# Optimization experiments

Hardware: AMD Instinct MI355X
Metric: run time of the kernel (lower is better)

The kernel has to match this reference:

```python
import jax, jax.numpy as jnp
import numpy as np
import math

L, H, P = 16384, 128, 256


def setup_inputs() -> dict:
    key = jax.random.key(0)
    k = jax.random.split(key, 6)
    return {
        "input_sequence": jax.random.normal(k[0], (L, H), dtype=jnp.float32),
        "A_diag": jax.random.uniform(k[1], (P,), dtype=jnp.float32),
        "B": (jax.random.uniform(k[2], (P, H, 2), dtype=jnp.float32) * 2.0 - 1.0) / math.sqrt(H),
        "C": (jax.random.uniform(k[3], (H, P, 2), dtype=jnp.float32) * 2.0 - 1.0) / math.sqrt(P),
        "D": jax.random.normal(k[4], (H,), dtype=jnp.float32),
        "steps": jax.random.uniform(k[5], (P,), dtype=jnp.float32),
    }


def _binop(qi, qj):
    # 2x2 block-diagonal matrix product + affine state propagation, per channel.
    iA, iB, iC, iD, ib1, ib2 = qi
    jA, jB, jC, jD, jb1, jb2 = qj
    return (
        jA * iA + jB * iC,
        jA * iB + jB * iD,
        jC * iA + jD * iC,
        jC * iB + jD * iD,
        jA * ib1 + jB * ib2 + jb1,
        jC * ib1 + jD * ib2 + jb2,
    )


def reference(input_sequence, A_diag, B, C, D, steps):
    # LinOSS-IM discretization (implicit)
    A = jax.nn.relu(A_diag)                      # (P,)
    dt = jax.nn.sigmoid(steps)                   # (P,)
    Bc = B[..., 0] + 1j * B[..., 1]              # (P,H) complex64
    Cc = C[..., 0] + 1j * C[..., 1]              # (H,P) complex64

    Bu = input_sequence @ Bc.T                   # (L,P) complex64

    schur = 1.0 / (1.0 + dt ** 2 * A)
    M11 = 1.0 - dt ** 2 * A * schur
    M12 = -dt * A * schur
    M21 = dt * schur
    M22 = schur

    ones = jnp.ones((input_sequence.shape[0], A.shape[0]), dtype=input_sequence.dtype)
    F1 = M11 * Bu * dt                           # (L,P) complex
    F2 = M21 * Bu * dt

    elems = (M11 * ones, M12 * ones, M21 * ones, M22 * ones, F1, F2)
    _, _, _, _, _, x2 = jax.lax.associative_scan(_binop, elems)  # scan over L

    ys = jnp.real(x2 @ Cc.T)                     # (L,H)
    return ys + input_sequence * D
```

## Files before the change

kernel.cpp:

```cpp
#include <hip/hip_runtime.h>
#include <hip/hip_bf16.h>
#include <math.h>

#define L 16384
#define H 128
#define P 256
#define CL 32
#define NCH (L/CL)
#define GS 16
#define NG (NCH/GS)
#define KDIM 512
#define NBU 512

typedef __attribute__((ext_vector_type(8))) short short8;
typedef __attribute__((ext_vector_type(4))) float f32x4;

__device__ inline unsigned short f2bf(float f){
  union { float f; unsigned u; } v; v.f = f;
  unsigned u = v.u;
  u += 0x7fffu + ((u >> 16) & 1u);
  return (unsigned short)(u >> 16);
}
__device__ inline float bf2f(unsigned short s){
  union { unsigned u; float f; } v; v.u = ((unsigned)s) << 16;
  return v.f;
}

struct Params { float M11,M12,M21,M22,s1,s2; };

__device__ inline Params get_params(const float* A_diag, const float* steps, int p){
  float A = A_diag[p]; A = A > 0.f ? A : 0.f;
  float dt = 1.f/(1.f + expf(-steps[p]));
  float schur = 1.f/(1.f + dt*dt*A);
  Params q;
  q.M11 = 1.f - dt*dt*A*schur;
  q.M12 = -dt*A*schur;
  q.M21 = dt*schur;
  q.M22 = schur;
  q.s1 = q.M11*dt;
  q.s2 = q.M21*dt;
  return q;
}

__global__ __launch_bounds__(256) void cast_in(const float* __restrict__ in,
                                               unsigned short* __restrict__ inb){
  int i = blockIdx.x * 256 + threadIdx.x;
  const float4* g = (const float4*)in;
  float4 a = g[i*2], b = g[i*2+1];
  union { short8 s; unsigned short u[8]; } o;
  o.u[0]=f2bf(a.x); o.u[1]=f2bf(a.y); o.u[2]=f2bf(a.z); o.u[3]=f2bf(a.w);
  o.u[4]=f2bf(b.x); o.u[5]=f2bf(b.y); o.u[6]=f2bf(b.z); o.u[7]=f2bf(b.w);
  ((short8*)inb)[i] = o.s;
}

__global__ __launch_bounds__(512) void bwswz_prep(const float* __restrict__ B,
                                                  unsigned short* __restrict__ BWswz){
  int k = blockIdx.x;
  int n = threadIdx.x;
  int p = n & 255, c = n >> 8;
  float v = B[((size_t)p*H + k)*2 + c];
  BWswz[((size_t)(k>>3)*NBU + n)*8 + (k&7)] = f2bf(v);
}

__global__ __launch_bounds__(128) void bswz_prep(const float* __restrict__ C,
                                                 unsigned short* __restrict__ Bswz){
  int k = blockIdx.x;
  int n = threadIdx.x;
  float v = (k < P) ? C[((size_t)n*P + k)*2]
                    : -C[((size_t)n*P + (k-P))*2 + 1];
  Bswz[((size_t)(k>>3)*H + n)*8 + (k&7)] = f2bf(v);
}

__device__ inline void chunk_bu_to_lds(int c, const short* __restrict__ inb,
                                       const short* __restrict__ BWswz,
                                       unsigned short (*sBu)[NBU+8]){
  int tid = threadIdx.x;
  int lane = tid & 63, w = tid >> 6;
  int ml = lane & 15, quad = lane >> 4;
  int mt = w & 1, ng = w >> 1;
  int lm0 = mt*16;
  const short* aptr = inb + (size_t)(c*CL + lm0 + ml)*H + quad*8;
  short8 av[4];
  #pragma unroll
  for (int ks=0; ks<4; ks++) av[ks] = *(const short8*)(aptr + ks*32);
  f32x4 acc[8];
  #pragma unroll
  for (int t=0;t<8;t++) acc[t] = (f32x4){0.f,0.f,0.f,0.f};
  #pragma unroll
  for (int ks=0; ks<4; ks++){
    #pragma unroll
    for (int t=0;t<8;t++){
      int n0 = (ng*8 + t)*16;
      short8 bv = *(const short8*)(BWswz + ((size_t)(ks*4+quad)*NBU + n0 + ml)*8);
      acc[t] = __builtin_amdgcn_mfma_f32_16x16x32_bf16(av[ks], bv, acc[t], 0, 0, 0);
    }
  }
  #pragma unroll
  for (int t=0;t<8;t++){
    int n = (ng*8+t)*16 + ml;
    #pragma unroll
    for (int r=0;r<4;r++)
      sBu[lm0 + quad*4 + r][n] = f2bf(acc[t][r]);
  }
}

__global__ __launch_bounds__(512) void bu_finals(const short* __restrict__ inb,
                                                 const short* __restrict__ BWswz,
                                                 const float* __restrict__ A_diag,
                                                 const float* __restrict__ steps,
                                                 float* __restrict__ finals){
  __shared__ unsigned short sBu[CL][NBU+8];
  int c = blockIdx.x;
  chunk_bu_to_lds(c, inb, BWswz, sBu);
  __syncthreads();
  int tid = threadIdx.x;
  int p = tid & 255, part = tid >> 8;
  Params q = get_params(A_diag, steps, p);
  float x1=0.f, x2=0.f;
  #pragma unroll
  for (int i=0;i<CL;i++){
    float u = bf2f(sBu[i][part*256 + p]);
    float n1 = q.M11*x1 + q.M12*x2 + q.s1*u;
    float n2 = q.M21*x1 + q.M22*x2 + q.s2*u;
    x1 = n1; x2 = n2;
  }
  ((float2*)finals)[(size_t)(part*NCH + c)*P + p] = make_float2(x1,x2);
}

__global__ __launch_bounds__(512) void group_scan(const float* __restrict__ A_diag,
                                                  const float* __restrict__ steps,
                                                  float* zf,
                                                  float* __restrict__ gfin){
  int tid = threadIdx.x;
  int p = tid & (P-1);
  int part = tid >> 8;
  int g = blockIdx.x;
  Params q = get_params(A_diag, steps, p);
  float a=q.M11, b=q.M12, c=q.M21, d=q.M22;
  #pragma unroll
  for (int s=0;s<5;s++){
    float na=a*a+b*c, nb=a*b+b*d, nc=c*a+d*c, nd=c*b+d*d;
    a=na;b=nb;c=nc;d=nd;
  }
  float2* z2 = (float2*)zf;
  float x1=0.f, x2=0.f;
  #pragma unroll
  for (int i=0;i<GS;i++){
    size_t idx = (size_t)(part*NCH + g*GS + i)*P + p;
    float2 f = z2[idx];
    z2[idx] = make_float2(x1,x2);
    float n1 = a*x1 + b*x2 + f.x;
    float n2 = c*x1 + d*x2 + f.y;
    x1=n1; x2=n2;
  }
  ((float2*)gfin)[(size_t)(part*NG + g)*P + p] = make_float2(x1,x2);
}

__global__ __launch_bounds__(512) void group_combine(const float* __restrict__ A_diag,
                                                     const float* __restrict__ steps,
                                                     const float* __restrict__ gfin,
                                                     float* __restrict__ Yarr){
  int tid = threadIdx.x;
  int p = tid & (P-1);
  int part = tid >> 8;
  Params q = get_params(A_diag, steps, p);
  float a=q.M11, b=q.M12, c=q.M21, d=q.M22;
  #pragma unroll
  for (int s=0;s<9;s++){
    float na=a*a+b*c, nb=a*b+b*d, nc=c*a+d*c, nd=c*b+d*d;
    a=na;b=nb;c=nc;d=nd;
  }
  const float2* Z2 = (const float2*)gfin;
  float2* Y2 = (float2*)Yarr;
  float x1=0.f, x2=0.f;
  #pragma unroll
  for (int g=0; g<NG; g++){
    size_t idx = (size_t)(part*NG + g)*P + p;
    Y2[idx] = make_float2(x1,x2);
    float2 z = Z2[idx];
    float n1 = a*x1 + b*x2 + z.x;
    float n2 = c*x1 + d*x2 + z.y;
    x1=n1; x2=n2;
  }
}

__global__ __launch_bounds__(512) void fused_out(const short* __restrict__ inb,
                                                 const short* __restrict__ BWswz,
                                                 const short* __restrict__ Bswz,
                                                 const float* __restrict__ A_diag,
                                                 const float* __restrict__ steps,
                                                 const float* __restrict__ zloc,
                                                 const float* __restrict__ Yarr,
                                                 const float* __restrict__ Dv,
                                                 const float* __restrict__ in,
                                                 float* __restrict__ out){
  __shared__ unsigned short sX[CL][KDIM+8];
  int c = blockIdx.x;
  chunk_bu_to_lds(c, inb, BWswz, sX);
  __syncthreads();

  int tid = threadIdx.x;
  {
    int p = tid & 255, part = tid >> 8;
    int g = c >> 4, iw = c & (GS-1);
    Params q = get_params(A_diag, steps, p);
    float a=q.M11, b=q.M12, cc=q.M21, dd=q.M22;
    #pragma unroll
    for (int s=0;s<5;s++){
      float na=a*a+b*cc, nb=a*b+b*dd, nc=cc*a+dd*cc, nd=cc*b+dd*dd;
      a=na;b=nb;cc=nc;dd=nd;
    }
    float sa=1.f, sb=0.f, sc=0.f, sd=1.f;
    float wa=a, wb=b, wc=cc, wd=dd;
    #pragma unroll
    for (int bit=0; bit<4; bit++){
      if ((iw>>bit)&1){
        float na = wa*sa + wb*sc, nb = wa*sb + wb*sd;
        float nc = wc*sa + wd*sc, nd = wc*sb + wd*sd;
        sa=na; sb=nb; sc=nc; sd=nd;
      }
      float qa = wa*wa + wb*wc, qb = wa*wb + wb*wd;
      float qc = wc*wa + wd*wc, qd = wc*wb + wd*wd;
      wa=qa; wb=qb; wc=qc; wd=qd;
    }
    float2 Y = ((const float2*)Yarr)[(size_t)(part*NG + g)*P + p];
    float2 z = ((const float2*)zloc)[(size_t)(part*NCH + c)*P + p];
    float x1 = sa*Y.x + sb*Y.y + z.x;
    float x2 = sc*Y.x + sd*Y.y + z.y;
    #pragma unroll
    for (int i=0;i<CL;i++){
      float u = bf2f(sX[i][part*256 + p]);
      float n1 = q.M11*x1 + q.M12*x2 + q.s1*u;
      float n2 = q.M21*x1 + q.M22*x2 + q.s2*u;
      x1 = n1; x2 = n2;
      sX[i][part*256 + p] = f2bf(x2);
    }
  }
  __syncthreads();

  int lane = tid & 63, w = tid >> 6;
  int ml = lane & 15, quad = lane >> 4;
  int mt = w & 1;
  int ntb = (w >> 1) * 2;
  f32x4 acc[2];
  acc[0] = (f32x4){0.f,0.f,0.f,0.f};
  acc[1] = (f32x4){0.f,0.f,0.f,0.f};
  for (int ks=0; ks<KDIM/32; ks++){
    short8 av = *(const short8*)&sX[mt*16 + ml][ks*32 + quad*8];
    #pragma unroll
    for (int j=0;j<2;j++){
      short8 bv = *(const short8*)(Bswz + ((size_t)(ks*4+quad)*H + (ntb+j)*16 + ml)*8);
      acc[j] = __builtin_amdgcn_mfma_f32_16x16x32_bf16(av, bv, acc[j], 0, 0, 0);
    }
  }
  #pragma unroll
  for (int j=0;j<2;j++){
    int h = (ntb+j)*16 + ml;
    float dv = Dv[h];
    #pragma unroll
    for (int r=0;r<4;r++){
      int l = c*CL + mt*16 + quad*4 + r;
      out[(size_t)l*H + h] = acc[j][r] + in[(size_t)l*H + h]*dv;
    }
  }
}

extern "C" void kernel_launch(void* const* d_in, const int* in_sizes, int n_in,
                              void* d_out, int out_size, void* d_ws, size_t ws_size,
                              hipStream_t stream) {
  const float* in     = (const float*)d_in[0];
  const float* A_diag = (const float*)d_in[1];
  const float* B      = (const float*)d_in[2];
  const float* Cw     = (const float*)d_in[3];
  const float* Dv     = (const float*)d_in[4];
  const float* steps  = (const float*)d_in[5];
  float* out = (float*)d_out;

  unsigned short* inb  = (unsigned short*)d_ws;
  unsigned short* BWswz= inb + (size_t)L*H;
  unsigned short* Bswz = BWswz + (size_t)H*NBU;
  float* finals = (float*)(Bswz + (size_t)KDIM*H);
  float* gfin   = finals + (size_t)2*NCH*P*2;
  float* Yarr   = gfin + (size_t)2*NG*P*2;

  cast_in<<<(L*H)/(8*256), 256, 0, stream>>>(in, inb);
  bwswz_prep<<<H, 512, 0, stream>>>(B, BWswz);
  bswz_prep<<<KDIM, 128, 0, stream>>>(Cw, Bswz);
  bu_finals<<<NCH, 512, 0, stream>>>((const short*)inb, (const short*)BWswz,
                                     A_diag, steps, finals);
  group_scan<<<NG, 512, 0, stream>>>(A_diag, steps, finals, gfin);
  group_combine<<<1, 512, 0, stream>>>(A_diag, steps, gfin, Yarr);
  fused_out<<<NCH, 512, 0, stream>>>((const short*)inb, (const short*)BWswz,
                                     (const short*)Bswz, A_diag, steps,
                                     finals, Yarr, Dv, in, out);
}
```

Before: 109.2 us.

## Merge all stages into one cooperative persistent kernel with grid syncs

Replaces the seven separate launches (cast/prep, chunk finals, group scan, group combine, fused output) with a single cooperative kernel that separates the phases with grid.sync(). The Bu tile stays in LDS between the chunk-finals phase and the output phase, so the output phase no longer recomputes the Bu GEMM. It also removes per-launch gaps. The trade-off is that 512 blocks of 512 threads must all be co-resident for the cooperative launch to succeed, and grid-wide barriers add cost. If the launch fails, the old multi-kernel path runs instead.

Result: slower. 325.5 us (+198.1%).

```diff
diff --git a/kernel.cpp b/kernel.cpp
--- a/kernel.cpp
+++ b/kernel.cpp
@@ -1,6 +1,8 @@
 #include <hip/hip_runtime.h>
-#include <hip/hip_bf16.h>
+#include <hip/hip_cooperative_groups.h>
 #include <math.h>
+
+namespace cg = cooperative_groups;
 
 #define L 16384
 #define H 128
@@ -42,6 +44,208 @@
   return q;
 }
 
+__device__ inline void chunk_bu_to_lds(int c, const short* __restrict__ inb,
+                                       const short* __restrict__ BWswz,
+                                       unsigned short (*sBu)[NBU+8]){
+  int tid = threadIdx.x;
+  int lane = tid & 63, w = tid >> 6;
+  int ml = lane & 15, quad = lane >> 4;
+  int mt = w & 1, ng = w >> 1;
+  int lm0 = mt*16;
+  const short* aptr = inb + (size_t)(c*CL + lm0 + ml)*H + quad*8;
+  short8 av[4];
+  #pragma unroll
+  for (int ks=0; ks<4; ks++) av[ks] = *(const short8*)(aptr + ks*32);
+  f32x4 acc[8];
+  #pragma unroll
+  for (int t=0;t<8;t++) acc[t] = (f32x4){0.f,0.f,0.f,0.f};
+  #pragma unroll
+  for (int ks=0; ks<4; ks++){
+    #pragma unroll
+    for (int t=0;t<8;t++){
+      int n0 = (ng*8 + t)*16;
+      short8 bv = *(const short8*)(BWswz + ((size_t)(ks*4+quad)*NBU + n0 + ml)*8);
+      acc[t] = __builtin_amdgcn_mfma_f32_16x16x32_bf16(av[ks], bv, acc[t], 0, 0, 0);
+    }
+  }
+  #pragma unroll
+  for (int t=0;t<8;t++){
+    int n = (ng*8+t)*16 + ml;
+    #pragma unroll
+    for (int r=0;r<4;r++)
+      sBu[lm0 + quad*4 + r][n] = f2bf(acc[t][r]);
+  }
+}
+
+__global__ __launch_bounds__(512, 4) void linoss_mega(
+    const float* __restrict__ in, const float* __restrict__ A_diag,
+    const float* __restrict__ B, const float* __restrict__ Cw,
+    const float* __restrict__ Dv, const float* __restrict__ steps,
+    unsigned short* __restrict__ inb, unsigned short* __restrict__ BWswz,
+    unsigned short* __restrict__ Bswz, float* finals,
+    float* __restrict__ gfin, float* __restrict__ Yarr,
+    float* __restrict__ out){
+  cg::grid_group grid = cg::this_grid();
+  __shared__ unsigned short sX[CL][NBU+8];
+  int tid = threadIdx.x;
+  int c = blockIdx.x;
+
+  {
+    int gid = c*512 + tid;
+    const float4* g = (const float4*)in;
+    float4 a = g[gid*2], b4 = g[gid*2+1];
+    union { short8 s; unsigned short u[8]; } o;
+    o.u[0]=f2bf(a.x); o.u[1]=f2bf(a.y); o.u[2]=f2bf(a.z); o.u[3]=f2bf(a.w);
+    o.u[4]=f2bf(b4.x); o.u[5]=f2bf(b4.y); o.u[6]=f2bf(b4.z); o.u[7]=f2bf(b4.w);
+    ((short8*)inb)[gid] = o.s;
+    if (gid < H*NBU){
+      int k = gid >> 9, n = gid & 511;
+      int p = n & 255, c2 = n >> 8;
+      float v = B[((size_t)p*H + k)*2 + c2];
+      BWswz[((size_t)(k>>3)*NBU + n)*8 + (k&7)] = f2bf(v);
+    }
+    if (gid < KDIM*H){
+      int k = gid >> 7, n = gid & 127;
+      float v = (k < P) ? Cw[((size_t)n*P + k)*2]
+                        : -Cw[((size_t)n*P + (k-P))*2 + 1];
+      Bswz[((size_t)(k>>3)*H + n)*8 + (k&7)] = f2bf(v);
+    }
+  }
+  grid.sync();
+
+  chunk_bu_to_lds(c, (const short*)inb, (const short*)BWswz, sX);
+  __syncthreads();
+  {
+    int p = tid & 255, part = tid >> 8;
+    Params q = get_params(A_diag, steps, p);
+    float x1=0.f, x2=0.f;
+    #pragma unroll
+    for (int i=0;i<CL;i++){
+      float u = bf2f(sX[i][part*256 + p]);
+      float n1 = q.M11*x1 + q.M12*x2 + q.s1*u;
+      float n2 = q.M21*x1 + q.M22*x2 + q.s2*u;
+      x1 = n1; x2 = n2;
+    }
+    ((float2*)finals)[(size_t)(part*NCH + c)*P + p] = make_float2(x1,x2);
+  }
+  grid.sync();
+
+  if (c < NG){
+    int p = tid & 255, part = tid >> 8;
+    int g = c;
+    Params q = get_params(A_diag, steps, p);
+    float a=q.M11, b=q.M12, cc=q.M21, d=q.M22;
+    #pragma unroll
+    for (int s=0;s<5;s++){
+      float na=a*a+b*cc, nb=a*b+b*d, nc=cc*a+d*cc, nd=cc*b+d*d;
+      a=na;b=nb;cc=nc;d=nd;
+    }
+    float2* z2 = (float2*)finals;
+    float x1=0.f, x2=0.f;
+    #pragma unroll
+    for (int i=0;i<GS;i++){
+      size_t idx = (size_t)(part*NCH + g*GS + i)*P + p;
+      float2 f = z2[idx];
+      z2[idx] = make_float2(x1,x2);
+      float n1 = a*x1 + b*x2 + f.x;
+      float n2 = cc*x1 + d*x2 + f.y;
+      x1=n1; x2=n2;
+    }
+    ((float2*)gfin)[(size_t)(part*NG + g)*P + p] = make_float2(x1,x2);
+  }
+  grid.sync();
+
+  if (c == 0){
+    int p = tid & 255, part = tid >> 8;
+    Params q = get_params(A_diag, steps, p);
+    float a=q.M11, b=q.M12, cc=q.M21, d=q.M22;
+    #pragma unroll
+    for (int s=0;s<9;s++){
+      float na=a*a+b*cc, nb=a*b+b*d, nc=cc*a+d*cc, nd=cc*b+d*d;
+      a=na;b=nb;cc=nc;d=nd;
+    }
+    const float2* Z2 = (const float2*)gfin;
+    float2* Y2 = (float2*)Yarr;
+    float x1=0.f, x2=0.f;
+    #pragma unroll
+    for (int g=0; g<NG; g++){
+      size_t idx = (size_t)(part*NG + g)*P + p;
+      Y2[idx] = make_float2(x1,x2);
+      float2 z = Z2[idx];
+      float n1 = a*x1 + b*x2 + z.x;
+      float n2 = cc*x1 + d*x2 + z.y;
+      x1=n1; x2=n2;
+    }
+  }
+  grid.sync();
+
+  {
+    int p = tid & 255, part = tid >> 8;
+    int g = c >> 4, iw = c & (GS-1);
+    Params q = get_params(A_diag, steps, p);
+    float a=q.M11, b=q.M12, cc=q.M21, dd=q.M22;
+    #pragma unroll
+    for (int s=0;s<5;s++){
+      float na=a*a+b*cc, nb=a*b+b*dd, nc=cc*a+dd*cc, nd=cc*b+dd*dd;
+      a=na;b=nb;cc=nc;dd=nd;
+    }
+    float sa=1.f, sb=0.f, sc=0.f, sd=1.f;
+    float wa=a, wb=b, wc=cc, wd=dd;
+    #pragma unroll
+    for (int bit=0; bit<4; bit++){
+      if ((iw>>bit)&1){
+        float na = wa*sa + wb*sc, nb = wa*sb + wb*sd;
+        float nc = wc*sa + wd*sc, nd = wc*sb + wd*sd;
+        sa=na; sb=nb; sc=nc; sd=nd;
+      }
+      float qa = wa*wa + wb*wc, qb = wa*wb + wb*wd;
+      float qc = wc*wa + wd*wc, qd = wc*wb + wd*wd;
+      wa=qa; wb=qb; wc=qc; wd=qd;
+    }
+    float2 Y = ((const float2*)Yarr)[(size_t)(part*NG + g)*P + p];
+    float2 z = ((const float2*)finals)[(size_t)(part*NCH + c)*P + p];
+    float x1 = sa*Y.x + sb*Y.y + z.x;
+    float x2 = sc*Y.x + sd*Y.y + z.y;
+    #pragma unroll
+    for (int i=0;i<CL;i++){
+      float u = bf2f(sX[i][part*256 + p]);
+      float n1 = q.M11*x1 + q.M12*x2 + q.s1*u;
+      float n2 = q.M21*x1 + q.M22*x2 + q.s2*u;
+      x1 = n1; x2 = n2;
+      sX[i][part*256 + p] = f2bf(x2);
+    }
+  }
+  __syncthreads();
+  {
+    int lane = tid & 63, w = tid >> 6;
+    int ml = lane & 15, quad = lane >> 4;
+    int mt = w & 1;
+    int ntb = (w >> 1) * 2;
+    f32x4 acc[2];
+    acc[0] = (f32x4){0.f,0.f,0.f,0.f};
+    acc[1] = (f32x4){0.f,0.f,0.f,0.f};
+    for (int ks=0; ks<KDIM/32; ks++){
+      short8 av = *(const short8*)&sX[mt*16 + ml][ks*32 + quad*8];
+      #pragma unroll
+      for (int j=0;j<2;j++){
+        short8 bv = *(const short8*)((const short*)Bswz +
+                      ((size_t)(ks*4+quad)*H + (ntb+j)*16 + ml)*8);
+        acc[j] = __builtin_amdgcn_mfma_f32_16x16x32_bf16(av, bv, acc[j], 0, 0, 0);
+      }
+    }
+    #pragma unroll
+    for (int j=0;j<2;j++){
+      int h = (ntb+j)*16 + ml;
+      float dv = Dv[h];
+      #pragma unroll
+      for (int r=0;r<4;r++){
+        int l = c*CL + mt*16 + quad*4 + r;
+        out[(size_t)l*H + h] = acc[j][r] + in[(size_t)l*H + h]*dv;
+      }
+    }
+  }
+}
+
 __global__ __launch_bounds__(256) void cast_in(const float* __restrict__ in,
                                                unsigned short* __restrict__ inb){
   int i = blockIdx.x * 256 + threadIdx.x;
@@ -69,39 +273,6 @@
   float v = (k < P) ? C[((size_t)n*P + k)*2]
                     : -C[((size_t)n*P + (k-P))*2 + 1];
   Bswz[((size_t)(k>>3)*H + n)*8 + (k&7)] = f2bf(v);
-}
-
-__device__ inline void chunk_bu_to_lds(int c, const short* __restrict__ inb,
-                                       const short* __restrict__ BWswz,
-                                       unsigned short (*sBu)[NBU+8]){
-  int tid = threadIdx.x;
-  int lane = tid & 63, w = tid >> 6;
-  int ml = lane & 15, quad = lane >> 4;
-  int mt = w & 1, ng = w >> 1;
-  int lm0 = mt*16;
-  const short* aptr = inb + (size_t)(c*CL + lm0 + ml)*H + quad*8;
-  short8 av[4];
-  #pragma unroll
-  for (int ks=0; ks<4; ks++) av[ks] = *(const short8*)(aptr + ks*32);
-  f32x4 acc[8];
-  #pragma unroll
-  for (int t=0;t<8;t++) acc[t] = (f32x4){0.f,0.f,0.f,0.f};
-  #pragma unroll
-  for (int ks=0; ks<4; ks++){
-    #pragma unroll
-    for (int t=0;t<8;t++){
-      int n0 = (ng*8 + t)*16;
-      short8 bv = *(const short8*)(BWswz + ((size_t)(ks*4+quad)*NBU + n0 + ml)*8);
-      acc[t] = __builtin_amdgcn_mfma_f32_16x16x32_bf16(av[ks], bv, acc[t], 0, 0, 0);
-    }
-  }
-  #pragma unroll
-  for (int t=0;t<8;t++){
-    int n = (ng*8+t)*16 + ml;
-    #pragma unroll
-    for (int r=0;r<4;r++)
-      sBu[lm0 + quad*4 + r][n] = f2bf(acc[t][r]);
-  }
 }
 
 __global__ __launch_bounds__(512) void bu_finals(const short* __restrict__ inb,
@@ -198,7 +369,6 @@
   int c = blockIdx.x;
   chunk_bu_to_lds(c, inb, BWswz, sX);
   __syncthreads();
-
   int tid = threadIdx.x;
   {
     int p = tid & 255, part = tid >> 8;
@@ -237,7 +407,6 @@
     }
   }
   __syncthreads();
-
   int lane = tid & 63, w = tid >> 6;
   int ml = lane & 15, quad = lane >> 4;
   int mt = w & 1;
@@ -283,14 +452,24 @@
   float* gfin   = finals + (size_t)2*NCH*P*2;
   float* Yarr   = gfin + (size_t)2*NG*P*2;
 
-  cast_in<<<(L*H)/(8*256), 256, 0, stream>>>(in, inb);
-  bwswz_prep<<<H, 512, 0, stream>>>(B, BWswz);
-  bswz_prep<<<KDIM, 128, 0, stream>>>(Cw, Bswz);
-  bu_finals<<<NCH, 512, 0, stream>>>((const short*)inb, (const short*)BWswz,
-                                     A_diag, steps, finals);
-  group_scan<<<NG, 512, 0, stream>>>(A_diag, steps, finals, gfin);
-  group_combine<<<1, 512, 0, stream>>>(A_diag, steps, gfin, Yarr);
-  fused_out<<<NCH, 512, 0, stream>>>((const short*)inb, (const short*)BWswz,
-                                     (const short*)Bswz, A_diag, steps,
-                                     finals, Yarr, Dv, in, out);
-}
+  void* args[] = {
+    (void*)&in, (void*)&A_diag, (void*)&B, (void*)&Cw, (void*)&Dv, (void*)&steps,
+    (void*)&inb, (void*)&BWswz, (void*)&Bswz,
+    (void*)&finals, (void*)&gfin, (void*)&Yarr, (void*)&out
+  };
+  hipError_t err = hipLaunchCooperativeKernel((const void*)linoss_mega,
+                                              dim3(NCH), dim3(512),
+                                              args, 0, stream);
+  if (err != hipSuccess) {
+    cast_in<<<(L*H)/(8*256), 256, 0, stream>>>(in, inb);
+    bwswz_prep<<<H, 512, 0, stream>>>(B, BWswz);
+    bswz_prep<<<KDIM, 128, 0, stream>>>(Cw, Bswz);
+    bu_finals<<<NCH, 512, 0, stream>>>((const short*)inb, (const short*)BWswz,
+                                       A_diag, steps, finals);
+    group_scan<<<NG, 512, 0, stream>>>(A_diag, steps, finals, gfin);
+    group_combine<<<1, 512, 0, stream>>>(A_diag, steps, gfin, Yarr);
+    fused_out<<<NCH, 512, 0, stream>>>((const short*)inb, (const short*)BWswz,
+                                       (const short*)Bswz, A_diag, steps,
+                                       finals, Yarr, Dv, in, out);
+  }
+}
```

## Merge prep kernels into one launch and fold group combine into output kernel

Applied to the files above, without the earlier changes.

Combines the three preparation kernels (input cast, B swizzle, C swizzle) into a single launch with 512 blocks. It also drops the single-block group_combine kernel. Each block of fused_out now recomputes its group carry-in by serially scanning up to 31 group finals with the 16th power of the transition matrix. This cuts two launches and removes a serial single-block kernel, at the cost of redundant per-block scan work and extra global reads in fused_out.

Result: faster. 104.3 us (-4.4%).

```diff
diff --git a/kernel.cpp b/kernel.cpp
--- a/kernel.cpp
+++ b/kernel.cpp
@@ -1,5 +1,4 @@
 #include <hip/hip_runtime.h>
-#include <hip/hip_bf16.h>
 #include <math.h>
 
 #define L 16384
@@ -42,33 +41,31 @@
   return q;
 }
 
-__global__ __launch_bounds__(256) void cast_in(const float* __restrict__ in,
-                                               unsigned short* __restrict__ inb){
-  int i = blockIdx.x * 256 + threadIdx.x;
+__global__ __launch_bounds__(512) void prep_all(const float* __restrict__ in,
+                                                const float* __restrict__ B,
+                                                const float* __restrict__ Cw,
+                                                unsigned short* __restrict__ inb,
+                                                unsigned short* __restrict__ BWswz,
+                                                unsigned short* __restrict__ Bswz){
+  int gid = blockIdx.x*512 + threadIdx.x;
   const float4* g = (const float4*)in;
-  float4 a = g[i*2], b = g[i*2+1];
+  float4 a = g[gid*2], b4 = g[gid*2+1];
   union { short8 s; unsigned short u[8]; } o;
   o.u[0]=f2bf(a.x); o.u[1]=f2bf(a.y); o.u[2]=f2bf(a.z); o.u[3]=f2bf(a.w);
-  o.u[4]=f2bf(b.x); o.u[5]=f2bf(b.y); o.u[6]=f2bf(b.z); o.u[7]=f2bf(b.w);
-  ((short8*)inb)[i] = o.s;
-}
-
-__global__ __launch_bounds__(512) void bwswz_prep(const float* __restrict__ B,
-                                                  unsigned short* __restrict__ BWswz){
-  int k = blockIdx.x;
-  int n = threadIdx.x;
-  int p = n & 255, c = n >> 8;
-  float v = B[((size_t)p*H + k)*2 + c];
-  BWswz[((size_t)(k>>3)*NBU + n)*8 + (k&7)] = f2bf(v);
-}
-
-__global__ __launch_bounds__(128) void bswz_prep(const float* __restrict__ C,
-                                                 unsigned short* __restrict__ Bswz){
-  int k = blockIdx.x;
-  int n = threadIdx.x;
-  float v = (k < P) ? C[((size_t)n*P + k)*2]
-                    : -C[((size_t)n*P + (k-P))*2 + 1];
-  Bswz[((size_t)(k>>3)*H + n)*8 + (k&7)] = f2bf(v);
+  o.u[4]=f2bf(b4.x); o.u[5]=f2bf(b4.y); o.u[6]=f2bf(b4.z); o.u[7]=f2bf(b4.w);
+  ((short8*)inb)[gid] = o.s;
+  if (gid < H*NBU){
+    int k = gid >> 9, n = gid & 511;
+    int p = n & 255, c2 = n >> 8;
+    float v = B[((size_t)p*H + k)*2 + c2];
+    BWswz[((size_t)(k>>3)*NBU + n)*8 + (k&7)] = f2bf(v);
+  }
+  if (gid < KDIM*H){
+    int k = gid >> 7, n = gid & 127;
+    float v = (k < P) ? Cw[((size_t)n*P + k)*2]
+                      : -Cw[((size_t)n*P + (k-P))*2 + 1];
+    Bswz[((size_t)(k>>3)*H + n)*8 + (k&7)] = f2bf(v);
+  }
 }
 
 __device__ inline void chunk_bu_to_lds(int c, const short* __restrict__ inb,
@@ -156,41 +153,13 @@
   ((float2*)gfin)[(size_t)(part*NG + g)*P + p] = make_float2(x1,x2);
 }
 
-__global__ __launch_bounds__(512) void group_combine(const float* __restrict__ A_diag,
-                                                     const float* __restrict__ steps,
-                                                     const float* __restrict__ gfin,
-                                                     float* __restrict__ Yarr){
-  int tid = threadIdx.x;
-  int p = tid & (P-1);
-  int part = tid >> 8;
-  Params q = get_params(A_diag, steps, p);
-  float a=q.M11, b=q.M12, c=q.M21, d=q.M22;
-  #pragma unroll
-  for (int s=0;s<9;s++){
-    float na=a*a+b*c, nb=a*b+b*d, nc=c*a+d*c, nd=c*b+d*d;
-    a=na;b=nb;c=nc;d=nd;
-  }
-  const float2* Z2 = (const float2*)gfin;
-  float2* Y2 = (float2*)Yarr;
-  float x1=0.f, x2=0.f;
-  #pragma unroll
-  for (int g=0; g<NG; g++){
-    size_t idx = (size_t)(part*NG + g)*P + p;
-    Y2[idx] = make_float2(x1,x2);
-    float2 z = Z2[idx];
-    float n1 = a*x1 + b*x2 + z.x;
-    float n2 = c*x1 + d*x2 + z.y;
-    x1=n1; x2=n2;
-  }
-}
-
 __global__ __launch_bounds__(512) void fused_out(const short* __restrict__ inb,
                                                  const short* __restrict__ BWswz,
                                                  const short* __restrict__ Bswz,
                                                  const float* __restrict__ A_diag,
                                                  const float* __restrict__ steps,
                                                  const float* __restrict__ zloc,
-                                                 const float* __restrict__ Yarr,
+                                                 const float* __restrict__ gfin,
                                                  const float* __restrict__ Dv,
                                                  const float* __restrict__ in,
                                                  float* __restrict__ out){
@@ -211,22 +180,37 @@
       a=na;b=nb;cc=nc;dd=nd;
     }
     float sa=1.f, sb=0.f, sc=0.f, sd=1.f;
-    float wa=a, wb=b, wc=cc, wd=dd;
-    #pragma unroll
-    for (int bit=0; bit<4; bit++){
-      if ((iw>>bit)&1){
-        float na = wa*sa + wb*sc, nb = wa*sb + wb*sd;
-        float nc = wc*sa + wd*sc, nd = wc*sb + wd*sd;
-        sa=na; sb=nb; sc=nc; sd=nd;
+    {
+      float wa=a, wb=b, wc=cc, wd=dd;
+      #pragma unroll
+      for (int bit=0; bit<4; bit++){
+        if ((iw>>bit)&1){
+          float na = wa*sa + wb*sc, nb = wa*sb + wb*sd;
+          float nc = wc*sa + wd*sc, nd = wc*sb + wd*sd;
+          sa=na; sb=nb; sc=nc; sd=nd;
+        }
+        float qa = wa*wa + wb*wc, qb = wa*wb + wb*wd;
+        float qc = wc*wa + wd*wc, qd = wc*wb + wd*wd;
+        wa=qa; wb=qb; wc=qc; wd=qd;
       }
-      float qa = wa*wa + wb*wc, qb = wa*wb + wb*wd;
-      float qc = wc*wa + wd*wc, qd = wc*wb + wd*wd;
-      wa=qa; wb=qb; wc=qc; wd=qd;
-    }
-    float2 Y = ((const float2*)Yarr)[(size_t)(part*NG + g)*P + p];
-    float2 z = ((const float2*)zloc)[(size_t)(part*NCH + c)*P + p];
-    float x1 = sa*Y.x + sb*Y.y + z.x;
-    float x2 = sc*Y.x + sd*Y.y + z.y;
+    }
+    float ga=a, gb=b, gc=cc, gd=dd;
+    #pragma unroll
+    for (int s=0;s<4;s++){
+      float na=ga*ga+gb*gc, nb=ga*gb+gb*gd, nc=gc*ga+gd*gc, nd=gc*gb+gd*gd;
+      ga=na;gb=nb;gc=nc;gd=nd;
+    }
+    float y1=0.f, y2=0.f;
+    const float2* Z2 = (const float2*)gfin;
+    for (int j=0; j<g; j++){
+      float2 z = Z2[(size_t)(part*NG + j)*P + p];
+      float n1 = ga*y1 + gb*y2 + z.x;
+      float n2 = gc*y1 + gd*y2 + z.y;
+      y1=n1; y2=n2;
+    }
+    float2 zc = ((const float2*)zloc)[(size_t)(part*NCH + c)*P + p];
+    float x1 = sa*y1 + sb*y2 + zc.x;
+    float x2 = sc*y1 + sd*y2 + zc.y;
     #pragma unroll
     for (int i=0;i<CL;i++){
       float u = bf2f(sX[i][part*256 + p]);
@@ -281,16 +265,12 @@
   unsigned short* Bswz = BWswz + (size_t)H*NBU;
   float* finals = (float*)(Bswz + (size_t)KDIM*H);
   float* gfin   = finals + (size_t)2*NCH*P*2;
-  float* Yarr   = gfin + (size_t)2*NG*P*2;
-
-  cast_in<<<(L*H)/(8*256), 256, 0, stream>>>(in, inb);
-  bwswz_prep<<<H, 512, 0, stream>>>(B, BWswz);
-  bswz_prep<<<KDIM, 128, 0, stream>>>(Cw, Bswz);
+
+  prep_all<<<512, 512, 0, stream>>>(in, B, Cw, inb, BWswz, Bswz);
   bu_finals<<<NCH, 512, 0, stream>>>((const short*)inb, (const short*)BWswz,
                                      A_diag, steps, finals);
   group_scan<<<NG, 512, 0, stream>>>(A_diag, steps, finals, gfin);
-  group_combine<<<1, 512, 0, stream>>>(A_diag, steps, gfin, Yarr);
   fused_out<<<NCH, 512, 0, stream>>>((const short*)inb, (const short*)BWswz,
                                      (const short*)Bswz, A_diag, steps,
-                                     finals, Yarr, Dv, in, out);
-}
+                                     finals, gfin, Dv, in, out);
+}
```
